# Optimization experiments

Hardware: AMD Instinct MI355X
Metric: run time of the kernel (lower is better)

## Reference

```python
import jax, jax.numpy as jnp
import numpy as np

N = 500_000          # number of tree nodes
K = 8                # attributes per group
ROWS, COLS = 2048, 4096   # image size; P = ROWS*COLS pixels


def _build_euler_tour(n, seed=0):
    """Random tree (parent[i] < i, parent[0] = 0) + real DFS Euler tour with a
    single timer incremented on both entry (tpre) and exit (tpost)."""
    rng = np.random.default_rng(seed)
    parent = np.zeros(n, dtype=np.int64)
    if n > 1:
        parent[1:] = np.floor(rng.random(n - 1) * np.arange(1, n)).astype(np.int64)
    counts = np.bincount(parent[1:], minlength=n)
    starts = np.zeros(n, dtype=np.int64)
    starts[1:] = np.cumsum(counts)[:-1]
    child_order = np.argsort(parent[1:], kind='stable') + 1  # children grouped by parent
    tpre = np.empty(n, dtype=np.int64)
    tpost = np.empty(n, dtype=np.int64)
    next_child = starts.copy()
    ends = starts + counts
    stack = np.empty(n, dtype=np.int64)
    sp = 0
    stack[0] = 0
    timer = 0
    tpre[0] = timer; timer += 1
    while sp >= 0:
        u = stack[sp]
        if next_child[u] < ends[u]:
            v = child_order[next_child[u]]
            next_child[u] += 1
            sp += 1
            stack[sp] = v
            tpre[v] = timer; timer += 1
        else:
            tpost[u] = timer; timer += 1
            sp -= 1
    return tpre, tpost


def setup_inputs() -> dict:
    key = jax.random.key(0)
    k1, k2, k3, k4 = jax.random.split(key, 4)
    tpre_np, tpost_np = _build_euler_tour(N)
    weight = jax.random.normal(k1, (K,), dtype=jnp.float32) * 0.1
    bias = jnp.zeros((1,), dtype=jnp.float32)
    residues = jax.random.normal(k2, (N,), dtype=jnp.float32)
    attrs2d = jax.random.uniform(k3, (N, K), dtype=jnp.float32)
    node_of_pixel = jax.random.randint(k4, (ROWS * COLS,), 0, N)
    return {
        'weight': weight,
        'bias': bias,
        'residues': residues,
        'attrs2d': attrs2d,
        'tpre': jnp.asarray(tpre_np),
        'tpost': jnp.asarray(tpost_np),
        'node_of_pixel': node_of_pixel,
        'numRows': ROWS,
        'numCols': COLS,
    }


def reference(weight, bias, residues, attrs2d, tpre, tpost, node_of_pixel, numRows, numCols):
    beta_f = 1.0  # module default; clamp_logits=False
    # logits = attrs2d @ w + b ; filtered residues per node
    logits = attrs2d @ weight + bias[0]                     # (N,)
    sig = jax.nn.sigmoid(beta_f * logits)                   # (N,)
    filtered = residues * sig                                # (N,)
    # implicit J.T @ filtered via Euler-tour scatter + prefix scan
    T = 2 * tpre.shape[0]                                    # tpost.max()+1 for a full DFS tour
    delta = (jnp.zeros((T,), dtype=filtered.dtype)
             .at[tpre].add(filtered)
             .at[tpost].add(-filtered))
    y_cumsum = jnp.cumsum(delta)                             # (2N,)
    y = y_cumsum[tpre[node_of_pixel]]                        # (P,) gather per pixel
    return y.reshape(numRows, numCols)
```

## Files before the change

### kernel.cpp

```cpp
#include <hip/hip_runtime.h>

typedef int   v4i __attribute__((ext_vector_type(4)));
typedef float v4f __attribute__((ext_vector_type(4)));

#define SCAN_THREADS 256
#define EPT 8
#define CHUNK (SCAN_THREADS * EPT)

#define NSEG   128
#define SEGLEN 8192
#define SCHUNK 1024

__device__ inline unsigned long long pack_sf(float v) {
    return (1ull << 32) | (unsigned long long)__float_as_uint(v);
}

__global__ void k1_filter_scatter(const float* __restrict__ attrs,
                                  const float* __restrict__ weight,
                                  const float* __restrict__ bias,
                                  const float* __restrict__ residues,
                                  const int* __restrict__ tpre,
                                  const int* __restrict__ tpost,
                                  float* __restrict__ delta, int N) {
    int u0 = (blockIdx.x * blockDim.x + threadIdx.x) * 2;
    v4f w0 = *(const v4f*)weight;
    v4f w1 = *(const v4f*)(weight + 4);
    float b = bias[0];
    if (u0 + 2 <= N) {
        float r0 = residues[u0], r1 = residues[u0 + 1];
        int pre0 = tpre[u0],  pre1 = tpre[u0 + 1];
        int pos0 = tpost[u0], pos1 = tpost[u0 + 1];
        v4f a00 = *(const v4f*)(attrs + (size_t)u0 * 8);
        v4f a01 = *(const v4f*)(attrs + (size_t)u0 * 8 + 4);
        v4f a10 = *(const v4f*)(attrs + (size_t)u0 * 8 + 8);
        v4f a11 = *(const v4f*)(attrs + (size_t)u0 * 8 + 12);
        float l0 = a00.x*w0.x + a00.y*w0.y + a00.z*w0.z + a00.w*w0.w +
                   a01.x*w1.x + a01.y*w1.y + a01.z*w1.z + a01.w*w1.w + b;
        float l1 = a10.x*w0.x + a10.y*w0.y + a10.z*w0.z + a10.w*w0.w +
                   a11.x*w1.x + a11.y*w1.y + a11.z*w1.z + a11.w*w1.w + b;
        float f0 = r0 / (1.0f + __expf(-l0));
        float f1 = r1 / (1.0f + __expf(-l1));
        delta[pre0] =  f0; delta[pre1] =  f1;
        delta[pos0] = -f0; delta[pos1] = -f1;
    } else {
        for (int u = u0; u < N; ++u) {
            float logit = b;
            #pragma unroll
            for (int k = 0; k < 8; ++k) logit += attrs[(size_t)u * 8 + k] * weight[k];
            float f = residues[u] / (1.0f + __expf(-logit));
            delta[tpre[u]]  =  f;
            delta[tpost[u]] = -f;
        }
    }
}

__global__ void __launch_bounds__(SCAN_THREADS)
scan128(float* __restrict__ data,
        unsigned long long* __restrict__ state, int T) {
    __shared__ float wavesums[SCAN_THREADS / 64];
    __shared__ float s_carry;
    const int seg  = blockIdx.x;
    const int base0 = seg * SEGLEN;
    const int segEnd = min(base0 + SEGLEN, T);
    const int lane = threadIdx.x & 63, wid = threadIdx.x >> 6;

    float acc = 0.0f;
    for (int off = base0 + threadIdx.x * 4; off < segEnd; off += SCHUNK) {
        if (off + 4 <= segEnd) {
            v4f v = *(const v4f*)(data + off);
            acc += v.x + v.y + v.z + v.w;
        } else {
            for (int i = 0; i < 4 && off + i < segEnd; ++i) acc += data[off + i];
        }
    }
    #pragma unroll
    for (int d = 32; d > 0; d >>= 1) acc += __shfl_down(acc, d, 64);
    if (lane == 0) wavesums[wid] = acc;
    __syncthreads();
    if (threadIdx.x == 0) {
        float segsum = wavesums[0] + wavesums[1] + wavesums[2] + wavesums[3];
        __hip_atomic_store(&state[seg], pack_sf(segsum), __ATOMIC_RELEASE,
                           __HIP_MEMORY_SCOPE_AGENT);
    }

    if (wid == 0) {
        float c = 0.0f;
        for (int i = lane; i < seg; i += 64) {
            unsigned long long p;
            do {
                p = __hip_atomic_load(&state[i], __ATOMIC_ACQUIRE,
                                      __HIP_MEMORY_SCOPE_AGENT);
            } while ((unsigned)(p >> 32) != 1u);
            c += __uint_as_float((unsigned)(p & 0xffffffffu));
        }
        #pragma unroll
        for (int d = 32; d > 0; d >>= 1) c += __shfl_down(c, d, 64);
        if (lane == 0) s_carry = c;
    }
    __syncthreads();
    float running = s_carry;

    for (int cb = base0; cb < segEnd; cb += SCHUNK) {
        int off = cb + threadIdx.x * 4;
        float v[4];
        bool full = (off + 4 <= segEnd);
        if (full) {
            v4f t = *(const v4f*)(data + off);
            v[0]=t.x; v[1]=t.y; v[2]=t.z; v[3]=t.w;
        } else {
            for (int i = 0; i < 4; ++i)
                v[i] = (off + i < segEnd) ? data[off + i] : 0.0f;
        }
        float run = 0.0f;
        #pragma unroll
        for (int i = 0; i < 4; ++i) { run += v[i]; v[i] = run; }
        float tot = run;
        float x = tot;
        #pragma unroll
        for (int d = 1; d < 64; d <<= 1) {
            float y = __shfl_up(x, d, 64);
            if (lane >= d) x += y;
        }
        if (lane == 63) wavesums[wid] = x;
        __syncthreads();
        float woff = 0.0f, chunktot = 0.0f;
        #pragma unroll
        for (int i = 0; i < SCAN_THREADS / 64; ++i) {
            if (i < wid) woff += wavesums[i];
            chunktot += wavesums[i];
        }
        float add = (x - tot) + woff + running;
        if (full) {
            v4f o = { v[0]+add, v[1]+add, v[2]+add, v[3]+add };
            *(v4f*)(data + off) = o;
        } else {
            for (int i = 0; i < 4; ++i)
                if (off + i < segEnd) data[off + i] = v[i] + add;
        }
        running += chunktot;
        __syncthreads();
    }
}

__global__ void k5_node_values(const float* __restrict__ ycum,
                               const int* __restrict__ tpre,
                               float* __restrict__ vnode, int N) {
    int u0 = (blockIdx.x * blockDim.x + threadIdx.x) * 2;
    if (u0 + 2 <= N) {
        int t0 = tpre[u0], t1 = tpre[u0 + 1];
        float y0 = ycum[t0], y1 = ycum[t1];
        vnode[u0] = y0; vnode[u0 + 1] = y1;
    } else {
        for (int u = u0; u < N; ++u) vnode[u] = ycum[tpre[u]];
    }
}

__global__ void k6_gather(const float* __restrict__ vnode,
                          const int* __restrict__ nop,
                          float* __restrict__ out, int P) {
    int i = (blockIdx.x * blockDim.x + threadIdx.x) * 4;
    if (i + 4 <= P) {
        v4i n = *(const v4i*)(nop + i);
        v4f o = { vnode[n.x], vnode[n.y], vnode[n.z], vnode[n.w] };
        *(v4f*)(out + i) = o;
    } else {
        for (; i < P; ++i) out[i] = vnode[nop[i]];
    }
}

__global__ void k2_partials(const float* __restrict__ delta,
                            float* __restrict__ partials, int T) {
    __shared__ float sdata[SCAN_THREADS / 64];
    int base = blockIdx.x * CHUNK + threadIdx.x * EPT;
    float s = 0.0f;
    if (base + EPT <= T) {
        v4f v0 = *(const v4f*)(delta + base);
        v4f v1 = *(const v4f*)(delta + base + 4);
        s = v0.x + v0.y + v0.z + v0.w + v1.x + v1.y + v1.z + v1.w;
    } else {
        for (int i = 0; i < EPT; ++i)
            if (base + i < T) s += delta[base + i];
    }
    #pragma unroll
    for (int d = 32; d > 0; d >>= 1) s += __shfl_down(s, d, 64);
    int lane = threadIdx.x & 63, wid = threadIdx.x >> 6;
    if (lane == 0) sdata[wid] = s;
    __syncthreads();
    if (threadIdx.x == 0)
        partials[blockIdx.x] = sdata[0] + sdata[1] + sdata[2] + sdata[3];
}

__global__ void k4_scan_chunks(float* __restrict__ data,
                               const float* __restrict__ partials, int T) {
    __shared__ float wavesums[SCAN_THREADS / 64];
    __shared__ float redsum[SCAN_THREADS / 64];
    int lane = threadIdx.x & 63, wid = threadIdx.x >> 6;
    float c = 0.0f;
    for (int i = threadIdx.x; i < blockIdx.x; i += SCAN_THREADS)
        c += partials[i];
    #pragma unroll
    for (int d = 32; d > 0; d >>= 1) c += __shfl_down(c, d, 64);
    if (lane == 0) redsum[wid] = c;
    int base = blockIdx.x * CHUNK + threadIdx.x * EPT;
    float v[EPT];
    bool full = (base + EPT <= T);
    if (full) {
        v4f v0 = *(const v4f*)(data + base);
        v4f v1 = *(const v4f*)(data + base + 4);
        v[0]=v0.x; v[1]=v0.y; v[2]=v0.z; v[3]=v0.w;
        v[4]=v1.x; v[5]=v1.y; v[6]=v1.z; v[7]=v1.w;
    } else {
        for (int i = 0; i < EPT; ++i)
            v[i] = (base + i < T) ? data[base + i] : 0.0f;
    }
    float run = 0.0f;
    #pragma unroll
    for (int i = 0; i < EPT; ++i) { run += v[i]; v[i] = run; }
    float tot = run;
    float x = tot;
    #pragma unroll
    for (int d = 1; d < 64; d <<= 1) {
        float y = __shfl_up(x, d, 64);
        if (lane >= d) x += y;
    }
    if (lane == 63) wavesums[wid] = x;
    __syncthreads();
    float woff = 0.0f, offset = redsum[0] + redsum[1] + redsum[2] + redsum[3];
    #pragma unroll
    for (int i = 0; i < SCAN_THREADS / 64; ++i)
        if (i < wid) woff += wavesums[i];
    float add = (x - tot) + woff + offset;
    if (full) {
        v4f o0 = { v[0]+add, v[1]+add, v[2]+add, v[3]+add };
        v4f o1 = { v[4]+add, v[5]+add, v[6]+add, v[7]+add };
        *(v4f*)(data + base)     = o0;
        *(v4f*)(data + base + 4) = o1;
    } else {
        for (int i = 0; i < EPT; ++i)
            if (base + i < T) data[base + i] = v[i] + add;
    }
}

extern "C" void kernel_launch(void* const* d_in, const int* in_sizes, int n_in,
                              void* d_out, int out_size, void* d_ws, size_t ws_size,
                              hipStream_t stream) {
    const float* weight   = (const float*)d_in[0];
    const float* bias     = (const float*)d_in[1];
    const float* residues = (const float*)d_in[2];
    const float* attrs    = (const float*)d_in[3];
    const int*   tpre     = (const int*)d_in[4];
    const int*   tpost    = (const int*)d_in[5];
    const int*   nop      = (const int*)d_in[6];
    float* out = (float*)d_out;

    const int N = in_sizes[2];
    const int T = 2 * N;
    const int P = out_size;

    size_t needMain = (size_t)(T + N) * sizeof(float) + NSEG * 8;
    size_t needMid  = (size_t)(N + 1024) * sizeof(float) + NSEG * 8;

    if (ws_size >= needMain) {
        float* delta = (float*)d_ws;
        float* vnode = delta + T;
        unsigned long long* state = (unsigned long long*)(vnode + N);
        k1_filter_scatter<<<(N / 2 + 255) / 256, 256, 0, stream>>>(
            attrs, weight, bias, residues, tpre, tpost, delta, N);
        scan128<<<NSEG, SCAN_THREADS, 0, stream>>>(delta, state, T);
        k5_node_values<<<(N / 2 + 255) / 256, 256, 0, stream>>>(delta, tpre, vnode, N);
        k6_gather<<<(P / 4 + 255) / 256, 256, 0, stream>>>(vnode, nop, out, P);
    } else {
        const int numChunks = (T + CHUNK - 1) / CHUNK;
        float *delta = out, *vnode = (float*)d_ws, *partials = vnode + N;
        k1_filter_scatter<<<(N / 2 + 255) / 256, 256, 0, stream>>>(
            attrs, weight, bias, residues, tpre, tpost, delta, N);
        k2_partials<<<numChunks, SCAN_THREADS, 0, stream>>>(delta, partials, T);
        k4_scan_chunks<<<numChunks, SCAN_THREADS, 0, stream>>>(delta, partials, T);
        k5_node_values<<<(N / 2 + 255) / 256, 256, 0, stream>>>(delta, tpre, vnode, N);
        k6_gather<<<(P / 4 + 255) / 256, 256, 0, stream>>>(vnode, nop, out, P);
    }
}
```

Before: 170.4 us.

## Scatter value/node pairs and fuse node-value extraction into single-pass scan

The scatter kernel now writes (filtered value, node id) pairs into the output buffer, which serves as scratch space, instead of a plain delta array. A new single-pass decoupled-lookback scan loads 16 pairs per thread and keeps them in registers. It scatters the inclusive prefix straight into the per-node value array for entry events, which removes the separate k5 gather kernel and the second read pass over the delta array. In exchange the scatter writes twice as many bytes, the scan does random writes into vnode, and the path depends on the output buffer being large enough to hold the pairs.

```diff
diff --git a/kernel.cpp b/kernel.cpp
--- a/kernel.cpp
+++ b/kernel.cpp
@@ -7,12 +7,141 @@
 #define EPT 8
 #define CHUNK (SCAN_THREADS * EPT)
 
-#define NSEG   128
-#define SEGLEN 8192
-#define SCHUNK 1024
-
-__device__ inline unsigned long long pack_sf(float v) {
-    return (1ull << 32) | (unsigned long long)__float_as_uint(v);
+#define PSEG     4096
+#define PTHREADS 256
+#define PPT      16
+
+__global__ void k1_pair_scatter(const float* __restrict__ attrs,
+                                const float* __restrict__ weight,
+                                const float* __restrict__ bias,
+                                const float* __restrict__ residues,
+                                const int* __restrict__ tpre,
+                                const int* __restrict__ tpost,
+                                int2* __restrict__ pairs, int N) {
+    int u0 = (blockIdx.x * blockDim.x + threadIdx.x) * 2;
+    v4f w0 = *(const v4f*)weight;
+    v4f w1 = *(const v4f*)(weight + 4);
+    float b = bias[0];
+    if (u0 + 2 <= N) {
+        float r0 = residues[u0], r1 = residues[u0 + 1];
+        int pre0 = tpre[u0],  pre1 = tpre[u0 + 1];
+        int pos0 = tpost[u0], pos1 = tpost[u0 + 1];
+        v4f a00 = *(const v4f*)(attrs + (size_t)u0 * 8);
+        v4f a01 = *(const v4f*)(attrs + (size_t)u0 * 8 + 4);
+        v4f a10 = *(const v4f*)(attrs + (size_t)u0 * 8 + 8);
+        v4f a11 = *(const v4f*)(attrs + (size_t)u0 * 8 + 12);
+        float l0 = a00.x*w0.x + a00.y*w0.y + a00.z*w0.z + a00.w*w0.w +
+                   a01.x*w1.x + a01.y*w1.y + a01.z*w1.z + a01.w*w1.w + b;
+        float l1 = a10.x*w0.x + a10.y*w0.y + a10.z*w0.z + a10.w*w0.w +
+                   a11.x*w1.x + a11.y*w1.y + a11.z*w1.z + a11.w*w1.w + b;
+        float f0 = r0 / (1.0f + __expf(-l0));
+        float f1 = r1 / (1.0f + __expf(-l1));
+        pairs[pre0] = { __float_as_int(f0),  u0 };
+        pairs[pre1] = { __float_as_int(f1),  u0 + 1 };
+        pairs[pos0] = { __float_as_int(-f0), ~u0 };
+        pairs[pos1] = { __float_as_int(-f1), ~(u0 + 1) };
+    } else {
+        for (int u = u0; u < N; ++u) {
+            float logit = b;
+            #pragma unroll
+            for (int k = 0; k < 8; ++k) logit += attrs[(size_t)u * 8 + k] * weight[k];
+            float f = residues[u] / (1.0f + __expf(-logit));
+            pairs[tpre[u]]  = { __float_as_int(f),  u };
+            pairs[tpost[u]] = { __float_as_int(-f), ~u };
+        }
+    }
+}
+
+__global__ void __launch_bounds__(PTHREADS)
+scan_pairs(const int* __restrict__ pairs,
+           float* __restrict__ vnode,
+           unsigned long long* __restrict__ state, int T) {
+    __shared__ float wavesums[PTHREADS / 64];
+    __shared__ float s_carry;
+    const int seg  = blockIdx.x;
+    const int lane = threadIdx.x & 63, wid = threadIdx.x >> 6;
+    const int tbase = seg * PSEG + threadIdx.x * PPT;
+
+    float f[PPT]; int idx[PPT];
+    #pragma unroll
+    for (int j = 0; j < PPT; j += 2) {
+        int p = tbase + j;
+        if (p + 2 <= T) {
+            v4i q = *(const v4i*)(pairs + 2 * (size_t)p);
+            f[j]     = __int_as_float(q.x); idx[j]     = q.y;
+            f[j + 1] = __int_as_float(q.z); idx[j + 1] = q.w;
+        } else {
+            #pragma unroll
+            for (int k = 0; k < 2; ++k) {
+                int pp = p + k;
+                if (pp < T) {
+                    int2 q = *(const int2*)(pairs + 2 * (size_t)pp);
+                    f[j + k] = __int_as_float(q.x); idx[j + k] = q.y;
+                } else { f[j + k] = 0.0f; idx[j + k] = -1; }
+            }
+        }
+    }
+
+    float run = 0.0f;
+    #pragma unroll
+    for (int j = 0; j < PPT; ++j) { run += f[j]; f[j] = run; }
+
+    float x = run;
+    #pragma unroll
+    for (int d = 1; d < 64; d <<= 1) {
+        float y = __shfl_up(x, d, 64);
+        if (lane >= d) x += y;
+    }
+    if (lane == 63) wavesums[wid] = x;
+    __syncthreads();
+    float woff = 0.0f, agg = 0.0f;
+    #pragma unroll
+    for (int i = 0; i < PTHREADS / 64; ++i) {
+        if (i < wid) woff += wavesums[i];
+        agg += wavesums[i];
+    }
+    float texcl = (x - run) + woff;
+
+    if (threadIdx.x == 0) {
+        unsigned long long p = (1ull << 32) |
+                               (unsigned long long)__float_as_uint(agg);
+        __hip_atomic_store(&state[seg], p, __ATOMIC_RELEASE,
+                           __HIP_MEMORY_SCOPE_AGENT);
+    }
+
+    if (wid == 0) {
+        float c = 0.0f;
+        for (int i = lane; i < seg; i += 64) {
+            unsigned long long p;
+            do {
+                p = __hip_atomic_load(&state[i], __ATOMIC_ACQUIRE,
+                                      __HIP_MEMORY_SCOPE_AGENT);
+            } while ((unsigned)(p >> 32) != 1u);
+            c += __uint_as_float((unsigned)(p & 0xffffffffu));
+        }
+        #pragma unroll
+        for (int d = 32; d > 0; d >>= 1) c += __shfl_down(c, d, 64);
+        if (lane == 0) s_carry = c;
+    }
+    __syncthreads();
+    float add = s_carry + texcl;
+
+    #pragma unroll
+    for (int j = 0; j < PPT; ++j)
+        if (idx[j] >= 0) vnode[idx[j]] = f[j] + add;
+}
+
+__global__ void k6_gather(const float* __restrict__ vnode,
+                          const int* __restrict__ nop,
+                          float* __restrict__ out, int P) {
+    int i = (blockIdx.x * blockDim.x + threadIdx.x) * 4;
+    if (i + 4 <= P) {
+        v4i n = *(const v4i*)(nop + i);
+        v4f o = { vnode[n.x], vnode[n.y], vnode[n.z], vnode[n.w] };
+        *(v4f*)(out + i) = o;
+    } else {
+        for (; i < P; ++i) out[i] = vnode[nop[i]];
+    }
 }
 
 __global__ void k1_filter_scatter(const float* __restrict__ attrs,
@@ -54,120 +183,6 @@
     }
 }
 
-__global__ void __launch_bounds__(SCAN_THREADS)
-scan128(float* __restrict__ data,
-        unsigned long long* __restrict__ state, int T) {
-    __shared__ float wavesums[SCAN_THREADS / 64];
-    __shared__ float s_carry;
-    const int seg  = blockIdx.x;
-    const int base0 = seg * SEGLEN;
-    const int segEnd = min(base0 + SEGLEN, T);
-    const int lane = threadIdx.x & 63, wid = threadIdx.x >> 6;
-
-    float acc = 0.0f;
-    for (int off = base0 + threadIdx.x * 4; off < segEnd; off += SCHUNK) {
-        if (off + 4 <= segEnd) {
-            v4f v = *(const v4f*)(data + off);
-            acc += v.x + v.y + v.z + v.w;
-        } else {
-            for (int i = 0; i < 4 && off + i < segEnd; ++i) acc += data[off + i];
-        }
-    }
-    #pragma unroll
-    for (int d = 32; d > 0; d >>= 1) acc += __shfl_down(acc, d, 64);
-    if (lane == 0) wavesums[wid] = acc;
-    __syncthreads();
-    if (threadIdx.x == 0) {
-        float segsum = wavesums[0] + wavesums[1] + wavesums[2] + wavesums[3];
-        __hip_atomic_store(&state[seg], pack_sf(segsum), __ATOMIC_RELEASE,
-                           __HIP_MEMORY_SCOPE_AGENT);
-    }
-
-    if (wid == 0) {
-        float c = 0.0f;
-        for (int i = lane; i < seg; i += 64) {
-            unsigned long long p;
-            do {
-                p = __hip_atomic_load(&state[i], __ATOMIC_ACQUIRE,
-                                      __HIP_MEMORY_SCOPE_AGENT);
-            } while ((unsigned)(p >> 32) != 1u);
-            c += __uint_as_float((unsigned)(p & 0xffffffffu));
-        }
-        #pragma unroll
-        for (int d = 32; d > 0; d >>= 1) c += __shfl_down(c, d, 64);
-        if (lane == 0) s_carry = c;
-    }
-    __syncthreads();
-    float running = s_carry;
-
-    for (int cb = base0; cb < segEnd; cb += SCHUNK) {
-        int off = cb + threadIdx.x * 4;
-        float v[4];
-        bool full = (off + 4 <= segEnd);
-        if (full) {
-            v4f t = *(const v4f*)(data + off);
-            v[0]=t.x; v[1]=t.y; v[2]=t.z; v[3]=t.w;
-        } else {
-            for (int i = 0; i < 4; ++i)
-                v[i] = (off + i < segEnd) ? data[off + i] : 0.0f;
-        }
-        float run = 0.0f;
-        #pragma unroll
-        for (int i = 0; i < 4; ++i) { run += v[i]; v[i] = run; }
-        float tot = run;
-        float x = tot;
-        #pragma unroll
-        for (int d = 1; d < 64; d <<= 1) {
-            float y = __shfl_up(x, d, 64);
-            if (lane >= d) x += y;
-        }
-        if (lane == 63) wavesums[wid] = x;
-        __syncthreads();
-        float woff = 0.0f, chunktot = 0.0f;
-        #pragma unroll
-        for (int i = 0; i < SCAN_THREADS / 64; ++i) {
-            if (i < wid) woff += wavesums[i];
-            chunktot += wavesums[i];
-        }
-        float add = (x - tot) + woff + running;
-        if (full) {
-            v4f o = { v[0]+add, v[1]+add, v[2]+add, v[3]+add };
-            *(v4f*)(data + off) = o;
-        } else {
-            for (int i = 0; i < 4; ++i)
-                if (off + i < segEnd) data[off + i] = v[i] + add;
-        }
-        running += chunktot;
-        __syncthreads();
-    }
-}
-
-__global__ void k5_node_values(const float* __restrict__ ycum,
-                               const int* __restrict__ tpre,
-                               float* __restrict__ vnode, int N) {
-    int u0 = (blockIdx.x * blockDim.x + threadIdx.x) * 2;
-    if (u0 + 2 <= N) {
-        int t0 = tpre[u0], t1 = tpre[u0 + 1];
-        float y0 = ycum[t0], y1 = ycum[t1];
-        vnode[u0] = y0; vnode[u0 + 1] = y1;
-    } else {
-        for (int u = u0; u < N; ++u) vnode[u] = ycum[tpre[u]];
-    }
-}
-
-__global__ void k6_gather(const float* __restrict__ vnode,
-                          const int* __restrict__ nop,
-                          float* __restrict__ out, int P) {
-    int i = (blockIdx.x * blockDim.x + threadIdx.x) * 4;
-    if (i + 4 <= P) {
-        v4i n = *(const v4i*)(nop + i);
-        v4f o = { vnode[n.x], vnode[n.y], vnode[n.z], vnode[n.w] };
-        *(v4f*)(out + i) = o;
-    } else {
-        for (; i < P; ++i) out[i] = vnode[nop[i]];
-    }
-}
-
 __global__ void k2_partials(const float* __restrict__ delta,
                             float* __restrict__ partials, int T) {
     __shared__ float sdata[SCAN_THREADS / 64];
@@ -238,6 +253,19 @@
     } else {
         for (int i = 0; i < EPT; ++i)
             if (base + i < T) data[base + i] = v[i] + add;
+    }
+}
+
+__global__ void k5_node_values(const float* __restrict__ ycum,
+                               const int* __restrict__ tpre,
+                               float* __restrict__ vnode, int N) {
+    int u0 = (blockIdx.x * blockDim.x + threadIdx.x) * 2;
+    if (u0 + 2 <= N) {
+        int t0 = tpre[u0], t1 = tpre[u0 + 1];
+        float y0 = ycum[t0], y1 = ycum[t1];
+        vnode[u0] = y0; vnode[u0 + 1] = y1;
+    } else {
+        for (int u = u0; u < N; ++u) vnode[u] = ycum[tpre[u]];
     }
 }
 
@@ -257,17 +285,20 @@
     const int T = 2 * N;
     const int P = out_size;
 
-    size_t needMain = (size_t)(T + N) * sizeof(float) + NSEG * 8;
-    size_t needMid  = (size_t)(N + 1024) * sizeof(float) + NSEG * 8;
-
-    if (ws_size >= needMain) {
-        float* delta = (float*)d_ws;
-        float* vnode = delta + T;
-        unsigned long long* state = (unsigned long long*)(vnode + N);
-        k1_filter_scatter<<<(N / 2 + 255) / 256, 256, 0, stream>>>(
-            attrs, weight, bias, residues, tpre, tpost, delta, N);
-        scan128<<<NSEG, SCAN_THREADS, 0, stream>>>(delta, state, T);
-        k5_node_values<<<(N / 2 + 255) / 256, 256, 0, stream>>>(delta, tpre, vnode, N);
+    const int numSegs = (T + PSEG - 1) / PSEG;
+
+    size_t needMain = (size_t)N * sizeof(float) + (size_t)numSegs * 8 + 64;
+    bool pairsFit = ((size_t)T * sizeof(int2)) <= (size_t)P * sizeof(float);
+
+    if (ws_size >= needMain && pairsFit && numSegs <= 256) {
+        float* vnode = (float*)d_ws;
+        unsigned long long* state =
+            (unsigned long long*)((char*)d_ws + ((size_t)N * 4 + 63) / 64 * 64);
+        int2* pairs = (int2*)d_out;
+        k1_pair_scatter<<<(N / 2 + 255) / 256, 256, 0, stream>>>(
+            attrs, weight, bias, residues, tpre, tpost, pairs, N);
+        scan_pairs<<<numSegs, PTHREADS, 0, stream>>>(
+            (const int*)pairs, vnode, state, T);
         k6_gather<<<(P / 4 + 255) / 256, 256, 0, stream>>>(vnode, nop, out, P);
     } else {
         const int numChunks = (T + CHUNK - 1) / CHUNK;
```

New measurement: 171.9 us. About the same (+0.9%).
